# Performance work log

Measured on AMD Instinct MI355X. Metric: run time of the kernel, lower is better.

## Reference

```python
import math
import jax, jax.numpy as jnp
import numpy as np

EPS = 1e-5
NUM_HEADER = 2


def pos_encoding(C, T, dtype):
    i = jnp.arange(C)
    exp = -((i - (i % 2)).astype(dtype) / C)
    freqs = jnp.power(jnp.asarray(10000.0, dtype), exp)[:, None]      # [C,1]
    phases = ((i % 2).astype(dtype) * (np.pi / 2))[:, None]           # [C,1]
    pos = jnp.arange(T, dtype=dtype)[None, :]                         # [1,T]
    return jnp.sin(pos * freqs + phases)                              # [C,T]


def layernorm2d(x, g, b):
    # LayerNorm over (C,T) jointly, per batch element (nn.LayerNorm([C, length]))
    mu = jnp.mean(x, axis=(1, 2), keepdims=True)
    var = jnp.mean((x - mu) ** 2, axis=(1, 2), keepdims=True)
    return (x - mu) * jax.lax.rsqrt(var + EPS) * g[None] + b[None]


def dsconv(x, dw_w, dw_b, pw_w, pw_b):
    # depthwise conv1d (groups=C, 'same' padding for odd k) + pointwise 1x1
    C = x.shape[1]
    k = dw_w.shape[-1]
    y = jax.lax.conv_general_dilated(
        x, dw_w[:, None, :], (1,), [(k // 2, k // 2)],
        dimension_numbers=('NCH', 'OIH', 'NCH'), feature_group_count=C)
    y = y + dw_b[None, :, None]
    y = jnp.einsum('bct,oc->bot', y, pw_w) + pw_b[None, :, None]
    return y


def attention(x, mask, Wq, Wk, Wv, Wo):
    # Faithful to source bug: all heads use Wqs[1]/Wks[1]/Wvs[1] -> identical heads.
    xt = jnp.transpose(x, (0, 2, 1))          # [B,T,C]
    C = xt.shape[-1]
    dk = C / NUM_HEADER
    q = xt @ Wq                               # [B,T,dk]
    k_ = xt @ Wk
    v = xt @ Wv
    s = jnp.einsum('bqd,bkd->bqk', q, k_) * (1.0 / math.sqrt(dk))
    hmask = mask[:, None, :]                  # mask over keys
    s = s * hmask + (1 - hmask) * (-1e30)
    a = jax.nn.softmax(s, axis=2) * mask[:, :, None]
    head = a @ v                              # [B,T,dk]
    heads = jnp.tile(head, (1, 1, NUM_HEADER))  # concat of identical heads
    out = heads @ Wo                          # [B,T,C]
    return jnp.transpose(out, (0, 2, 1))      # [B,C,T]


def setup_inputs() -> dict:
    key = jax.random.key(0)
    B, C, T = 16, 128, 1024
    NCONV, K = 4, 7
    dk = C // NUM_HEADER
    ks = jax.random.split(key, 12)
    inp = {
        'x': jax.random.normal(ks[0], (B, C, T), jnp.float32),
        'mask': jnp.ones((B, T), jnp.float32),
        'dw_w': jax.random.normal(ks[1], (NCONV, C, K), jnp.float32) * math.sqrt(2.0 / K),
        'dw_b': jnp.zeros((NCONV, C), jnp.float32),
        'pw_w': jax.random.normal(ks[2], (NCONV, C, C), jnp.float32) * math.sqrt(2.0 / C),
        'pw_b': jnp.zeros((NCONV, C), jnp.float32),
        'norm0_g': jnp.ones((C, T), jnp.float32),
        'norm0_b': jnp.zeros((C, T), jnp.float32),
        'norms_g': jnp.ones((NCONV, C, T), jnp.float32),
        'norms_b': jnp.zeros((NCONV, C, T), jnp.float32),
        'norme_g': jnp.ones((C, T), jnp.float32),
        'norme_b': jnp.zeros((C, T), jnp.float32),
        'Wq': jax.random.normal(ks[3], (C, dk), jnp.float32) * math.sqrt(2.0 / (C + dk)),
        'Wk': jax.random.normal(ks[4], (C, dk), jnp.float32) * math.sqrt(2.0 / (C + dk)),
        'Wv': jax.random.normal(ks[5], (C, dk), jnp.float32) * math.sqrt(2.0 / (C + dk)),
        'Wo': jax.random.normal(ks[6], (C, C), jnp.float32) * math.sqrt(2.0 / C),
        'fc_w': jax.random.normal(ks[7], (C, C), jnp.float32) * (0.1 * math.sqrt(6.0 / (2 * C))),
        'fc_b': jnp.zeros((C,), jnp.float32),
    }
    return inp


def reference(x, mask, dw_w, dw_b, pw_w, pw_b, norm0_g, norm0_b,
              norms_g, norms_b, norme_g, norme_b,
              Wq, Wk, Wv, Wo, fc_w, fc_b):
    B, C, T = x.shape
    nconv = dw_w.shape[0]
    # dropout is identity in eval mode (reference is deterministic)
    out = x + pos_encoding(C, T, x.dtype)[None]
    res = layernorm2d(out, norm0_g, norm0_b)
    for i in range(nconv):
        out = dsconv(out, dw_w[i], dw_b[i], pw_w[i], pw_b[i])
        out = jax.nn.relu(out)
        out = out + res
        res = out
        out = layernorm2d(out, norms_g[i], norms_b[i])
    out = attention(out, mask, Wq, Wk, Wv, Wo)
    out = out + res
    res = out
    out = layernorm2d(out, norme_g, norme_b)
    out = jnp.einsum('bct,oc->bot', out, fc_w) + fc_b[None, :, None]
    out = jax.nn.relu(out)
    out = out + res
    return out
```

## Files before the change

kernel.cpp:

```cpp
#include <hip/hip_runtime.h>
#include <math.h>

#define BB 16
#define CC 128
#define TT 1024
#define KK 7
#define DK 64
#define NSPLIT 4

typedef float f32x4 __attribute__((ext_vector_type(4)));
typedef short s16x8 __attribute__((ext_vector_type(8)));

__device__ inline short f2bf(float f) {
  union { float f; unsigned u; } v; v.f = f;
  unsigned r = (v.u + 0x7FFFu + ((v.u >> 16) & 1u)) >> 16;
  return (short)r;
}

__device__ inline void block_partial_256(float s, float ss, float* dst) {
#pragma unroll
  for (int off = 32; off; off >>= 1) { s += __shfl_xor(s, off); ss += __shfl_xor(ss, off); }
  __shared__ float red[8];
  int w = threadIdx.x >> 6;
  if ((threadIdx.x & 63) == 0) { red[2 * w] = s; red[2 * w + 1] = ss; }
  __syncthreads();
  if (threadIdx.x == 0) {
    for (int i = 1; i < 4; ++i) { s += red[2 * i]; ss += red[2 * i + 1]; }
    dst[0] = s; dst[1] = ss;
  }
}

__device__ inline void ln_stats_from_parts(const float* part_batch, int n, float* sh) {
  if (threadIdx.x < 64) {
    float s = 0.f, ss = 0.f;
    for (int i = threadIdx.x; i < n; i += 64) { s += part_batch[2 * i]; ss += part_batch[2 * i + 1]; }
#pragma unroll
    for (int off = 32; off; off >>= 1) { s += __shfl_xor(s, off); ss += __shfl_xor(ss, off); }
    if (threadIdx.x == 0) {
      const float invN = 1.f / (float)(CC * TT);
      float mu = s * invN;
      sh[0] = mu;
      sh[1] = rsqrtf(ss * invN - mu * mu + 1e-5f);
    }
  }
  __syncthreads();
}

__global__ __launch_bounds__(256) void k_prep(const float* __restrict__ pww,
                                              const float* __restrict__ Wq,
                                              const float* __restrict__ Wk,
                                              const float* __restrict__ Wv,
                                              const float* __restrict__ Wo,
                                              const float* __restrict__ fcw,
                                              short* __restrict__ pwwb,
                                              short* __restrict__ wqkvb,
                                              short* __restrict__ wo2b,
                                              short* __restrict__ fcwb) {
  int i = blockIdx.x * 256 + threadIdx.x;
  if (i < 65536) { pwwb[i] = f2bf(pww[i]); return; }
  i -= 65536;
  if (i < 24576) {
    int m = i >> 7, c = i & 127;
    int sel = m >> 6, d = m & 63;
    const float* srcp = sel == 0 ? Wq : (sel == 1 ? Wk : Wv);
    wqkvb[i] = f2bf(srcp[c * DK + d]);
    return;
  }
  i -= 24576;
  if (i < 8192) {
    int o = i >> 6, d = i & 63;
    wo2b[i] = f2bf(Wo[d * CC + o] + Wo[(d + 64) * CC + o]);
    return;
  }
  i -= 8192;
  fcwb[i] = f2bf(fcw[i]);
}

__global__ __launch_bounds__(256) void k_addpos(const float* __restrict__ x,
                                                float* __restrict__ out,
                                                float* __restrict__ part) {
  int bc = blockIdx.x;
  int c = bc & (CC - 1);
  float ce = (float)(c & ~1);
  float freq = expf(-(ce / (float)CC) * 9.210340371976184f);
  float phase = (c & 1) ? 1.5707963267948966f : 0.0f;
  const float* xr = x + (size_t)bc * TT;
  float* orow = out + (size_t)bc * TT;
  float s = 0.f, ss = 0.f;
  for (int t = threadIdx.x; t < TT; t += 256) {
    float v = xr[t] + sinf((float)t * freq + phase);
    orow[t] = v;
    s += v; ss += v * v;
  }
  block_partial_256(s, ss, part + (size_t)bc * 2);
}

template <bool LN_IN, bool LN_RES>
__global__ __launch_bounds__(256) void k_dsconv(const float* __restrict__ in,
                                                const float* __restrict__ lng,
                                                const float* __restrict__ lnb,
                                                const float* __restrict__ part_in, int npart,
                                                const float* __restrict__ dww,
                                                const float* __restrict__ dwb,
                                                const short* __restrict__ pwwb,
                                                const float* __restrict__ pwb,
                                                float* __restrict__ out,
                                                float* __restrict__ part_out) {
  int tile = blockIdx.x & 31, b = blockIdx.x >> 5;
  int t0 = tile * 32;
  __shared__ float stats[2];
  __shared__ float xs[CC][39];
  __shared__ __align__(16) short Dt[32][136];
  ln_stats_from_parts(part_in + (size_t)b * npart * 2, npart, stats);
  float mu = stats[0], rs = stats[1];

  for (int i = threadIdx.x; i < CC * 38; i += 256) {
    int c = i / 38, j = i - c * 38;
    int t = t0 + j - 3;
    float v = 0.f;
    if (t >= 0 && t < TT) {
      v = in[((size_t)b * CC + c) * TT + t];
      if (LN_IN) v = (v - mu) * rs * lng[c * TT + t] + lnb[c * TT + t];
    }
    xs[c][j] = v;
  }
  __syncthreads();
  for (int i = threadIdx.x; i < 32 * CC; i += 256) {
    int t = i >> 7, c = i & 127;
    float a = dwb[c];
#pragma unroll
    for (int j = 0; j < KK; ++j) a += dww[c * KK + j] * xs[c][t + j];
    Dt[t][c] = f2bf(a);
  }
  __syncthreads();

  int w = threadIdx.x >> 6, lane = threadIdx.x & 63;
  int lo = lane & 15, hi = lane >> 4;
  f32x4 acc[2][2];
#pragma unroll
  for (int mt = 0; mt < 2; ++mt)
#pragma unroll
    for (int nt = 0; nt < 2; ++nt) { acc[mt][nt][0] = 0.f; acc[mt][nt][1] = 0.f; acc[mt][nt][2] = 0.f; acc[mt][nt][3] = 0.f; }
#pragma unroll
  for (int ks = 0; ks < 4; ++ks) {
    s16x8 b0 = *(const s16x8*)&Dt[lo][ks * 32 + hi * 8];
    s16x8 b1 = *(const s16x8*)&Dt[16 + lo][ks * 32 + hi * 8];
    s16x8 a0 = *(const s16x8*)&pwwb[(size_t)(w * 32 + lo) * CC + ks * 32 + hi * 8];
    s16x8 a1 = *(const s16x8*)&pwwb[(size_t)(w * 32 + 16 + lo) * CC + ks * 32 + hi * 8];
    acc[0][0] = __builtin_amdgcn_mfma_f32_16x16x32_bf16(a0, b0, acc[0][0], 0, 0, 0);
    acc[0][1] = __builtin_amdgcn_mfma_f32_16x16x32_bf16(a0, b1, acc[0][1], 0, 0, 0);
    acc[1][0] = __builtin_amdgcn_mfma_f32_16x16x32_bf16(a1, b0, acc[1][0], 0, 0, 0);
    acc[1][1] = __builtin_amdgcn_mfma_f32_16x16x32_bf16(a1, b1, acc[1][1], 0, 0, 0);
  }

  float s = 0.f, ss = 0.f;
#pragma unroll
  for (int mt = 0; mt < 2; ++mt)
#pragma unroll
    for (int nt = 0; nt < 2; ++nt)
#pragma unroll
      for (int r = 0; r < 4; ++r) {
        int row = w * 32 + mt * 16 + hi * 4 + r;
        int t = t0 + nt * 16 + lo;
        float v = acc[mt][nt][r] + pwb[row];
        v = v > 0.f ? v : 0.f;
        size_t idx = ((size_t)b * CC + row) * TT + t;
        float rv = in[idx];
        if (LN_RES) rv = (rv - mu) * rs * lng[row * TT + t] + lnb[row * TT + t];
        v += rv;
        out[idx] = v;
        s += v; ss += v * v;
      }
  block_partial_256(s, ss, part_out + (size_t)blockIdx.x * 2);
}

__global__ __launch_bounds__(256) void k_qkv(const float* __restrict__ in,
                                             const float* __restrict__ lng,
                                             const float* __restrict__ lnb,
                                             const float* __restrict__ part_in,
                                             const short* __restrict__ wqkvb,
                                             short* __restrict__ q,
                                             short* __restrict__ k,
                                             short* __restrict__ vt) {
  int tile = blockIdx.x & 31, b = blockIdx.x >> 5;
  int t0 = tile * 32;
  __shared__ float stats[2];
  __shared__ __align__(16) short Dt[32][136];
  ln_stats_from_parts(part_in + (size_t)b * 64, 32, stats);
  float mu = stats[0], rs = stats[1];
  for (int i = threadIdx.x; i < CC * 32; i += 256) {
    int c = i >> 5, t = i & 31;
    float v = in[((size_t)b * CC + c) * TT + t0 + t];
    Dt[t][c] = f2bf((v - mu) * rs * lng[c * TT + t0 + t] + lnb[c * TT + t0 + t]);
  }
  __syncthreads();

  int w = threadIdx.x >> 6, lane = threadIdx.x & 63;
  int lo = lane & 15, hi = lane >> 4;
  f32x4 acc[3][2];
#pragma unroll
  for (int mt = 0; mt < 3; ++mt)
#pragma unroll
    for (int nt = 0; nt < 2; ++nt) { acc[mt][nt][0] = 0.f; acc[mt][nt][1] = 0.f; acc[mt][nt][2] = 0.f; acc[mt][nt][3] = 0.f; }
#pragma unroll
  for (int ks = 0; ks < 4; ++ks) {
    s16x8 b0 = *(const s16x8*)&Dt[lo][ks * 32 + hi * 8];
    s16x8 b1 = *(const s16x8*)&Dt[16 + lo][ks * 32 + hi * 8];
#pragma unroll
    for (int mt = 0; mt < 3; ++mt) {
      s16x8 a = *(const s16x8*)&wqkvb[(size_t)(w * 48 + mt * 16 + lo) * CC + ks * 32 + hi * 8];
      acc[mt][0] = __builtin_amdgcn_mfma_f32_16x16x32_bf16(a, b0, acc[mt][0], 0, 0, 0);
      acc[mt][1] = __builtin_amdgcn_mfma_f32_16x16x32_bf16(a, b1, acc[mt][1], 0, 0, 0);
    }
  }
#pragma unroll
  for (int mt = 0; mt < 3; ++mt)
#pragma unroll
    for (int nt = 0; nt < 2; ++nt) {
      int m0 = w * 48 + mt * 16 + hi * 4;
      int t = t0 + nt * 16 + lo;
      short4 pk;
      pk.x = f2bf(acc[mt][nt][0]); pk.y = f2bf(acc[mt][nt][1]);
      pk.z = f2bf(acc[mt][nt][2]); pk.w = f2bf(acc[mt][nt][3]);
      if (m0 < 64) {
        *(short4*)(q + ((size_t)b * TT + t) * DK + m0) = pk;
      } else if (m0 < 128) {
        *(short4*)(k + ((size_t)b * TT + t) * DK + (m0 - 64)) = pk;
      } else {
        int d = m0 - 128;
        vt[((size_t)b * DK + d) * TT + t] = pk.x;
        vt[((size_t)b * DK + d + 1) * TT + t] = pk.y;
        vt[((size_t)b * DK + d + 2) * TT + t] = pk.z;
        vt[((size_t)b * DK + d + 3) * TT + t] = pk.w;
      }
    }
}

__global__ __launch_bounds__(128) void k_attn(const short* __restrict__ qb,
                                              const short* __restrict__ kbuf,
                                              const short* __restrict__ vtb,
                                              const float* __restrict__ mask,
                                              float* __restrict__ pacc,
                                              float* __restrict__ pml) {
  int sp = blockIdx.x & (NSPLIT - 1);
  int qt = (blockIdx.x >> 2) & 31;
  int b = blockIdx.x >> 7;
  int w = threadIdx.x >> 6, lane = threadIdx.x & 63;
  int lo = lane & 15, hi = lane >> 4;

  __shared__ __align__(16) short ks[64][72];
  __shared__ __align__(16) short vt[64][72];
  __shared__ __align__(16) short ps[2][16][68];
  __shared__ float ms[64];

  const short* qp = qb + ((size_t)b * TT + qt * 32 + w * 16 + lo) * DK + hi * 8;
  s16x8 aq0 = *(const s16x8*)qp;
  s16x8 aq1 = *(const s16x8*)(qp + 32);

  f32x4 acc[4];
  float m_i[4], l_i[4];
#pragma unroll
  for (int r = 0; r < 4; ++r) {
    m_i[r] = -3.0e38f; l_i[r] = 0.f;
#pragma unroll
    for (int nt = 0; nt < 4; ++nt) acc[nt][r] = 0.f;
  }
  const float scale = 0.125f;

  for (int kb2 = sp * (TT / 64 / NSPLIT); kb2 < (sp + 1) * (TT / 64 / NSPLIT); ++kb2) {
    __syncthreads();
    for (int i = threadIdx.x; i < 512; i += 128) {
      int r = i >> 3, ch = i & 7;
      *(s16x8*)&ks[r][ch * 8] =
          *(const s16x8*)(kbuf + ((size_t)b * TT + kb2 * 64 + r) * DK + ch * 8);
      *(s16x8*)&vt[r][ch * 8] =
          *(const s16x8*)(vtb + ((size_t)b * DK + r) * TT + kb2 * 64 + ch * 8);
    }
    if (threadIdx.x < 64) ms[threadIdx.x] = mask[(size_t)b * TT + kb2 * 64 + threadIdx.x];
    __syncthreads();

    f32x4 sc[4];
#pragma unroll
    for (int nt = 0; nt < 4; ++nt) {
      f32x4 z; z[0] = 0.f; z[1] = 0.f; z[2] = 0.f; z[3] = 0.f;
      s16x8 bk0 = *(const s16x8*)&ks[nt * 16 + lo][hi * 8];
      s16x8 bk1 = *(const s16x8*)&ks[nt * 16 + lo][32 + hi * 8];
      z = __builtin_amdgcn_mfma_f32_16x16x32_bf16(aq0, bk0, z, 0, 0, 0);
      z = __builtin_amdgcn_mfma_f32_16x16x32_bf16(aq1, bk1, z, 0, 0, 0);
      sc[nt] = z;
    }
#pragma unroll
    for (int nt = 0; nt < 4; ++nt) {
      float mv = ms[nt * 16 + lo];
      float addv = (1.f - mv) * -1e30f;
#pragma unroll
      for (int r = 0; r < 4; ++r) sc[nt][r] = sc[nt][r] * scale * mv + addv;
    }
    float alpha[4];
#pragma unroll
    for (int r = 0; r < 4; ++r) {
      float m0 = fmaxf(fmaxf(sc[0][r], sc[1][r]), fmaxf(sc[2][r], sc[3][r]));
#pragma unroll
      for (int off = 1; off < 16; off <<= 1) m0 = fmaxf(m0, __shfl_xor(m0, off));
      float mn = fmaxf(m_i[r], m0);
      alpha[r] = __expf(m_i[r] - mn);
      m_i[r] = mn;
    }
    float psum[4] = {0.f, 0.f, 0.f, 0.f};
#pragma unroll
    for (int nt = 0; nt < 4; ++nt)
#pragma unroll
      for (int r = 0; r < 4; ++r) {
        float p = __expf(sc[nt][r] - m_i[r]);
        psum[r] += p;
        ps[w][hi * 4 + r][nt * 16 + lo] = f2bf(p);
      }
#pragma unroll
    for (int r = 0; r < 4; ++r) {
      float sum = psum[r];
#pragma unroll
      for (int off = 1; off < 16; off <<= 1) sum += __shfl_xor(sum, off);
      l_i[r] = l_i[r] * alpha[r] + sum;
    }
#pragma unroll
    for (int nt = 0; nt < 4; ++nt)
#pragma unroll
      for (int r = 0; r < 4; ++r) acc[nt][r] *= alpha[r];

    s16x8 ap0 = *(const s16x8*)&ps[w][lo][hi * 8];
    s16x8 ap1 = *(const s16x8*)&ps[w][lo][32 + hi * 8];
#pragma unroll
    for (int nt = 0; nt < 4; ++nt) {
      s16x8 bv0 = *(const s16x8*)&vt[nt * 16 + lo][hi * 8];
      s16x8 bv1 = *(const s16x8*)&vt[nt * 16 + lo][32 + hi * 8];
      acc[nt] = __builtin_amdgcn_mfma_f32_16x16x32_bf16(ap0, bv0, acc[nt], 0, 0, 0);
      acc[nt] = __builtin_amdgcn_mfma_f32_16x16x32_bf16(ap1, bv1, acc[nt], 0, 0, 0);
    }
  }
#pragma unroll
  for (int r = 0; r < 4; ++r) {
    int row = qt * 32 + w * 16 + hi * 4 + r;
    size_t pb = (((size_t)b * TT + row) * NSPLIT + sp) * DK;
#pragma unroll
    for (int nt = 0; nt < 4; ++nt) pacc[pb + nt * 16 + lo] = acc[nt][r];
    if (lo == 0) {
      size_t mb = (((size_t)b * TT + row) * NSPLIT + sp) * 2;
      pml[mb] = m_i[r];
      pml[mb + 1] = l_i[r];
    }
  }
}

__global__ __launch_bounds__(256) void k_attn_combine(const float* __restrict__ pacc,
                                                      const float* __restrict__ pml,
                                                      const float* __restrict__ mask,
                                                      short* __restrict__ head) {
  int tid = blockIdx.x * 256 + threadIdx.x;
  int chunk = tid & 3;
  int row = (tid >> 2) & (TT - 1);
  int b = tid >> 12;
  size_t rb = (size_t)b * TT + row;
  float m[NSPLIT], l[NSPLIT];
#pragma unroll
  for (int s = 0; s < NSPLIT; ++s) {
    m[s] = pml[(rb * NSPLIT + s) * 2];
    l[s] = pml[(rb * NSPLIT + s) * 2 + 1];
  }
  float M = fmaxf(fmaxf(m[0], m[1]), fmaxf(m[2], m[3]));
  float wgt[NSPLIT], L = 0.f;
#pragma unroll
  for (int s = 0; s < NSPLIT; ++s) { wgt[s] = __expf(m[s] - M); L += wgt[s] * l[s]; }
  float inv = mask[rb] / L;
  float o[16];
#pragma unroll
  for (int j = 0; j < 16; ++j) o[j] = 0.f;
#pragma unroll
  for (int s = 0; s < NSPLIT; ++s) {
    const float4* pa = (const float4*)(pacc + (rb * NSPLIT + s) * DK + chunk * 16);
#pragma unroll
    for (int j4 = 0; j4 < 4; ++j4) {
      float4 v = pa[j4];
      o[j4 * 4] += wgt[s] * v.x; o[j4 * 4 + 1] += wgt[s] * v.y;
      o[j4 * 4 + 2] += wgt[s] * v.z; o[j4 * 4 + 3] += wgt[s] * v.w;
    }
  }
  short h[16];
#pragma unroll
  for (int j = 0; j < 16; ++j) h[j] = f2bf(o[j] * inv);
  *(uint4*)(head + rb * DK + chunk * 16) = *(uint4*)h;
  *(uint4*)(head + rb * DK + chunk * 16 + 8) = *(uint4*)(h + 8);
}

__global__ __launch_bounds__(256) void k_attnout(const short* __restrict__ head,
                                                 const short* __restrict__ wo2b,
                                                 const float* __restrict__ res,
                                                 float* __restrict__ out,
                                                 float* __restrict__ part_out) {
  int tile = blockIdx.x & 31, b = blockIdx.x >> 5;
  int t0 = tile * 32;
  __shared__ __align__(16) short Ht[32][72];
  {
    int i = threadIdx.x;
    int t = i >> 3, ch = i & 7;
    *(s16x8*)&Ht[t][ch * 8] =
        *(const s16x8*)(head + ((size_t)b * TT + t0 + t) * DK + ch * 8);
  }
  __syncthreads();

  int w = threadIdx.x >> 6, lane = threadIdx.x & 63;
  int lo = lane & 15, hi = lane >> 4;
  f32x4 acc[2][2];
#pragma unroll
  for (int mt = 0; mt < 2; ++mt)
#pragma unroll
    for (int nt = 0; nt < 2; ++nt) { acc[mt][nt][0] = 0.f; acc[mt][nt][1] = 0.f; acc[mt][nt][2] = 0.f; acc[mt][nt][3] = 0.f; }
#pragma unroll
  for (int ks = 0; ks < 2; ++ks) {
    s16x8 b0 = *(const s16x8*)&Ht[lo][ks * 32 + hi * 8];
    s16x8 b1 = *(const s16x8*)&Ht[16 + lo][ks * 32 + hi * 8];
    s16x8 a0 = *(const s16x8*)&wo2b[(size_t)(w * 32 + lo) * DK + ks * 32 + hi * 8];
    s16x8 a1 = *(const s16x8*)&wo2b[(size_t)(w * 32 + 16 + lo) * DK + ks * 32 + hi * 8];
    acc[0][0] = __builtin_amdgcn_mfma_f32_16x16x32_bf16(a0, b0, acc[0][0], 0, 0, 0);
    acc[0][1] = __builtin_amdgcn_mfma_f32_16x16x32_bf16(a0, b1, acc[0][1], 0, 0, 0);
    acc[1][0] = __builtin_amdgcn_mfma_f32_16x16x32_bf16(a1, b0, acc[1][0], 0, 0, 0);
    acc[1][1] = __builtin_amdgcn_mfma_f32_16x16x32_bf16(a1, b1, acc[1][1], 0, 0, 0);
  }
  float s = 0.f, ss = 0.f;
#pragma unroll
  for (int mt = 0; mt < 2; ++mt)
#pragma unroll
    for (int nt = 0; nt < 2; ++nt)
#pragma unroll
      for (int r = 0; r < 4; ++r) {
        int row = w * 32 + mt * 16 + hi * 4 + r;
        int t = t0 + nt * 16 + lo;
        size_t idx = ((size_t)b * CC + row) * TT + t;
        float v = acc[mt][nt][r] + res[idx];
        out[idx] = v;
        s += v; ss += v * v;
      }
  block_partial_256(s, ss, part_out + (size_t)blockIdx.x * 2);
}

__global__ __launch_bounds__(256) void k_fc(const float* __restrict__ in,
                                            const float* __restrict__ lng,
                                            const float* __restrict__ lnb,
                                            const float* __restrict__ part_in,
                                            const short* __restrict__ fcwb,
                                            const float* __restrict__ fb,
                                            float* __restrict__ out) {
  int tile = blockIdx.x & 31, b = blockIdx.x >> 5;
  int t0 = tile * 32;
  __shared__ float stats[2];
  __shared__ __align__(16) short Dt[32][136];
  ln_stats_from_parts(part_in + (size_t)b * 64, 32, stats);
  float mu = stats[0], rs = stats[1];
  for (int i = threadIdx.x; i < CC * 32; i += 256) {
    int c = i >> 5, t = i & 31;
    float v = in[((size_t)b * CC + c) * TT + t0 + t];
    Dt[t][c] = f2bf((v - mu) * rs * lng[c * TT + t0 + t] + lnb[c * TT + t0 + t]);
  }
  __syncthreads();

  int w = threadIdx.x >> 6, lane = threadIdx.x & 63;
  int lo = lane & 15, hi = lane >> 4;
  f32x4 acc[2][2];
#pragma unroll
  for (int mt = 0; mt < 2; ++mt)
#pragma unroll
    for (int nt = 0; nt < 2; ++nt) { acc[mt][nt][0] = 0.f; acc[mt][nt][1] = 0.f; acc[mt][nt][2] = 0.f; acc[mt][nt][3] = 0.f; }
#pragma unroll
  for (int ks = 0; ks < 4; ++ks) {
    s16x8 b0 = *(const s16x8*)&Dt[lo][ks * 32 + hi * 8];
    s16x8 b1 = *(const s16x8*)&Dt[16 + lo][ks * 32 + hi * 8];
    s16x8 a0 = *(const s16x8*)&fcwb[(size_t)(w * 32 + lo) * CC + ks * 32 + hi * 8];
    s16x8 a1 = *(const s16x8*)&fcwb[(size_t)(w * 32 + 16 + lo) * CC + ks * 32 + hi * 8];
    acc[0][0] = __builtin_amdgcn_mfma_f32_16x16x32_bf16(a0, b0, acc[0][0], 0, 0, 0);
    acc[0][1] = __builtin_amdgcn_mfma_f32_16x16x32_bf16(a0, b1, acc[0][1], 0, 0, 0);
    acc[1][0] = __builtin_amdgcn_mfma_f32_16x16x32_bf16(a1, b0, acc[1][0], 0, 0, 0);
    acc[1][1] = __builtin_amdgcn_mfma_f32_16x16x32_bf16(a1, b1, acc[1][1], 0, 0, 0);
  }
#pragma unroll
  for (int mt = 0; mt < 2; ++mt)
#pragma unroll
    for (int nt = 0; nt < 2; ++nt)
#pragma unroll
      for (int r = 0; r < 4; ++r) {
        int row = w * 32 + mt * 16 + hi * 4 + r;
        int t = t0 + nt * 16 + lo;
        size_t idx = ((size_t)b * CC + row) * TT + t;
        float v = acc[mt][nt][r] + fb[row];
        v = v > 0.f ? v : 0.f;
        out[idx] = v + in[idx];
      }
}

extern "C" void kernel_launch(void* const* d_in, const int* in_sizes, int n_in,
                              void* d_out, int out_size, void* d_ws, size_t ws_size,
                              hipStream_t stream) {
  const float* x    = (const float*)d_in[0];
  const float* mask = (const float*)d_in[1];
  const float* dww  = (const float*)d_in[2];
  const float* dwb  = (const float*)d_in[3];
  const float* pww  = (const float*)d_in[4];
  const float* pwb  = (const float*)d_in[5];
  const float* n0g  = (const float*)d_in[6];
  const float* n0b  = (const float*)d_in[7];
  const float* nsg  = (const float*)d_in[8];
  const float* nsb  = (const float*)d_in[9];
  const float* neg_ = (const float*)d_in[10];
  const float* neb  = (const float*)d_in[11];
  const float* Wq   = (const float*)d_in[12];
  const float* Wk   = (const float*)d_in[13];
  const float* Wv   = (const float*)d_in[14];
  const float* Wo   = (const float*)d_in[15];
  const float* fcw  = (const float*)d_in[16];
  const float* fcb  = (const float*)d_in[17];
  float* out = (float*)d_out;

  float* W = (float*)d_ws;
  const size_t NBCT = (size_t)BB * CC * TT;
  const size_t NBTD = (size_t)BB * TT * DK;
  const size_t CT = (size_t)CC * TT;
  float* O     = W;
  float* S     = W + NBCT;
  float* PART0 = W + 2 * NBCT;
  float* PARTS = PART0 + 4096;
  float* PACC  = PARTS + 5 * 1024;
  float* PML   = PACC + NBTD * NSPLIT;
  short* QB    = (short*)(PML + (size_t)BB * TT * NSPLIT * 2);
  short* KB    = QB + NBTD;
  short* VT    = KB + NBTD;
  short* HDB   = VT + NBTD;
  short* PWWB  = HDB + NBTD;
  short* WQKVB = PWWB + 65536;
  short* WO2B  = WQKVB + 24576;
  short* FCWB  = WO2B + 8192;

  k_prep<<<448, 256, 0, stream>>>(pww, Wq, Wk, Wv, Wo, fcw, PWWB, WQKVB, WO2B, FCWB);
  k_addpos<<<BB * CC, 256, 0, stream>>>(x, O, PART0);
  k_dsconv<false, true><<<BB * 32, 256, 0, stream>>>(
      O, n0g, n0b, PART0, 128, dww, dwb, PWWB, pwb, S, PARTS);
  k_dsconv<true, false><<<BB * 32, 256, 0, stream>>>(
      S, nsg + 0 * CT, nsb + 0 * CT, PARTS, 32,
      dww + 1 * CC * KK, dwb + 1 * CC, PWWB + 1 * CC * CC, pwb + 1 * CC, O, PARTS + 1024);
  k_dsconv<true, false><<<BB * 32, 256, 0, stream>>>(
      O, nsg + 1 * CT, nsb + 1 * CT, PARTS + 1024, 32,
      dww + 2 * CC * KK, dwb + 2 * CC, PWWB + 2 * CC * CC, pwb + 2 * CC, S, PARTS + 2048);
  k_dsconv<true, false><<<BB * 32, 256, 0, stream>>>(
      S, nsg + 2 * CT, nsb + 2 * CT, PARTS + 2048, 32,
      dww + 3 * CC * KK, dwb + 3 * CC, PWWB + 3 * CC * CC, pwb + 3 * CC, O, PARTS + 3072);
  k_qkv<<<BB * 32, 256, 0, stream>>>(O, nsg + 3 * CT, nsb + 3 * CT, PARTS + 3072,
                                     WQKVB, QB, KB, VT);
  k_attn<<<BB * 32 * NSPLIT, 128, 0, stream>>>(QB, KB, VT, mask, PACC, PML);
  k_attn_combine<<<BB * TT * 4 / 256, 256, 0, stream>>>(PACC, PML, mask, HDB);
  k_attnout<<<BB * 32, 256, 0, stream>>>(HDB, WO2B, O, S, PARTS + 4096);
  k_fc<<<BB * 32, 256, 0, stream>>>(S, neg_, neb, PARTS + 4096, FCWB, fcb, out);
}
```

Baseline: 218.6 us.

## Store intermediates and LN params in bf16, fuse attention combine into output projection

Switches the inter-kernel activation buffers (O/S), the attention partial accumulators, and the per-element LayerNorm gamma/beta copies to bf16, halving global memory traffic in the bandwidth-bound conv/LN kernels. The split-K attention combine kernel is folded into the attention output projection kernel, removing a launch and one round trip through memory. The prep kernel now also converts the LN parameters on every call, which adds work, and the bf16 residual stream reduces accuracy.

```diff
diff --git a/kernel.cpp b/kernel.cpp
--- a/kernel.cpp
+++ b/kernel.cpp
@@ -16,6 +16,11 @@
   unsigned r = (v.u + 0x7FFFu + ((v.u >> 16) & 1u)) >> 16;
   return (short)r;
 }
+__device__ inline float bf2f(short s) {
+  union { unsigned u; float f; } v;
+  v.u = ((unsigned)(unsigned short)s) << 16;
+  return v.f;
+}
 
 __device__ inline void block_partial_256(float s, float ss, float* dst) {
 #pragma unroll
@@ -52,10 +57,17 @@
                                               const float* __restrict__ Wv,
                                               const float* __restrict__ Wo,
                                               const float* __restrict__ fcw,
+                                              const float* __restrict__ n0g,
+                                              const float* __restrict__ n0b,
+                                              const float* __restrict__ nsg,
+                                              const float* __restrict__ nsb,
+                                              const float* __restrict__ neg_,
+                                              const float* __restrict__ neb,
                                               short* __restrict__ pwwb,
                                               short* __restrict__ wqkvb,
                                               short* __restrict__ wo2b,
-                                              short* __restrict__ fcwb) {
+                                              short* __restrict__ fcwb,
+                                              short* __restrict__ lnpb) {
   int i = blockIdx.x * 256 + threadIdx.x;
   if (i < 65536) { pwwb[i] = f2bf(pww[i]); return; }
   i -= 65536;
@@ -73,38 +85,53 @@
     return;
   }
   i -= 8192;
-  fcwb[i] = f2bf(fcw[i]);
+  if (i < 16384) { fcwb[i] = f2bf(fcw[i]); return; }
+  i -= 16384;
+  if (i >= 1572864) return;
+  const int CT = CC * TT;
+  float v;
+  if (i < CT) v = n0g[i];
+  else if (i < 2 * CT) v = n0b[i - CT];
+  else if (i < 6 * CT) v = nsg[i - 2 * CT];
+  else if (i < 10 * CT) v = nsb[i - 6 * CT];
+  else if (i < 11 * CT) v = neg_[i - 10 * CT];
+  else v = neb[i - 11 * CT];
+  lnpb[i] = f2bf(v);
 }
 
 __global__ __launch_bounds__(256) void k_addpos(const float* __restrict__ x,
-                                                float* __restrict__ out,
+                                                short* __restrict__ out,
                                                 float* __restrict__ part) {
   int bc = blockIdx.x;
   int c = bc & (CC - 1);
   float ce = (float)(c & ~1);
   float freq = expf(-(ce / (float)CC) * 9.210340371976184f);
   float phase = (c & 1) ? 1.5707963267948966f : 0.0f;
-  const float* xr = x + (size_t)bc * TT;
-  float* orow = out + (size_t)bc * TT;
-  float s = 0.f, ss = 0.f;
-  for (int t = threadIdx.x; t < TT; t += 256) {
-    float v = xr[t] + sinf((float)t * freq + phase);
-    orow[t] = v;
-    s += v; ss += v * v;
-  }
+  const float4* xr = (const float4*)(x + (size_t)bc * TT);
+  short* orow = out + (size_t)bc * TT;
+  int t = threadIdx.x * 4;
+  float4 xv = xr[threadIdx.x];
+  float v0 = xv.x + sinf((float)t * freq + phase);
+  float v1 = xv.y + sinf((float)(t + 1) * freq + phase);
+  float v2 = xv.z + sinf((float)(t + 2) * freq + phase);
+  float v3 = xv.w + sinf((float)(t + 3) * freq + phase);
+  float s = v0 + v1 + v2 + v3;
+  float ss = v0 * v0 + v1 * v1 + v2 * v2 + v3 * v3;
+  short4 o; o.x = f2bf(v0); o.y = f2bf(v1); o.z = f2bf(v2); o.w = f2bf(v3);
+  *(short4*)(orow + t) = o;
   block_partial_256(s, ss, part + (size_t)bc * 2);
 }
 
 template <bool LN_IN, bool LN_RES>
-__global__ __launch_bounds__(256) void k_dsconv(const float* __restrict__ in,
-                                                const float* __restrict__ lng,
-                                                const float* __restrict__ lnb,
+__global__ __launch_bounds__(256) void k_dsconv(const short* __restrict__ in,
+                                                const short* __restrict__ lng,
+                                                const short* __restrict__ lnb,
                                                 const float* __restrict__ part_in, int npart,
                                                 const float* __restrict__ dww,
                                                 const float* __restrict__ dwb,
                                                 const short* __restrict__ pwwb,
                                                 const float* __restrict__ pwb,
-                                                float* __restrict__ out,
+                                                short* __restrict__ out,
                                                 float* __restrict__ part_out) {
   int tile = blockIdx.x & 31, b = blockIdx.x >> 5;
   int t0 = tile * 32;
@@ -119,8 +146,8 @@
     int t = t0 + j - 3;
     float v = 0.f;
     if (t >= 0 && t < TT) {
-      v = in[((size_t)b * CC + c) * TT + t];
-      if (LN_IN) v = (v - mu) * rs * lng[c * TT + t] + lnb[c * TT + t];
+      v = bf2f(in[((size_t)b * CC + c) * TT + t]);
+      if (LN_IN) v = (v - mu) * rs * bf2f(lng[c * TT + t]) + bf2f(lnb[c * TT + t]);
     }
     xs[c][j] = v;
   }
@@ -165,18 +192,18 @@
         float v = acc[mt][nt][r] + pwb[row];
         v = v > 0.f ? v : 0.f;
         size_t idx = ((size_t)b * CC + row) * TT + t;
-        float rv = in[idx];
-        if (LN_RES) rv = (rv - mu) * rs * lng[row * TT + t] + lnb[row * TT + t];
+        float rv = bf2f(in[idx]);
+        if (LN_RES) rv = (rv - mu) * rs * bf2f(lng[row * TT + t]) + bf2f(lnb[row * TT + t]);
         v += rv;
-        out[idx] = v;
+        out[idx] = f2bf(v);
         s += v; ss += v * v;
       }
   block_partial_256(s, ss, part_out + (size_t)blockIdx.x * 2);
 }
 
-__global__ __launch_bounds__(256) void k_qkv(const float* __restrict__ in,
-                                             const float* __restrict__ lng,
-                                             const float* __restrict__ lnb,
+__global__ __launch_bounds__(256) void k_qkv(const short* __restrict__ in,
+                                             const short* __restrict__ lng,
+                                             const short* __restrict__ lnb,
                                              const float* __restrict__ part_in,
                                              const short* __restrict__ wqkvb,
                                              short* __restrict__ q,
@@ -188,10 +215,16 @@
   __shared__ __align__(16) short Dt[32][136];
   ln_stats_from_parts(part_in + (size_t)b * 64, 32, stats);
   float mu = stats[0], rs = stats[1];
-  for (int i = threadIdx.x; i < CC * 32; i += 256) {
-    int c = i >> 5, t = i & 31;
-    float v = in[((size_t)b * CC + c) * TT + t0 + t];
-    Dt[t][c] = f2bf((v - mu) * rs * lng[c * TT + t0 + t] + lnb[c * TT + t0 + t]);
+  for (int i = threadIdx.x; i < CC * 16; i += 256) {
+    int c = i >> 4, t2 = (i & 15) * 2;
+    size_t base = ((size_t)b * CC + c) * TT + t0 + t2;
+    unsigned u = *(const unsigned*)(in + base);
+    unsigned g = *(const unsigned*)(lng + c * TT + t0 + t2);
+    unsigned bb2 = *(const unsigned*)(lnb + c * TT + t0 + t2);
+    float v0 = (bf2f((short)(u & 0xFFFF)) - mu) * rs * bf2f((short)(g & 0xFFFF)) + bf2f((short)(bb2 & 0xFFFF));
+    float v1 = (bf2f((short)(u >> 16)) - mu) * rs * bf2f((short)(g >> 16)) + bf2f((short)(bb2 >> 16));
+    Dt[t2][c] = f2bf(v0);
+    Dt[t2 + 1][c] = f2bf(v1);
   }
   __syncthreads();
 
@@ -240,7 +273,7 @@
                                               const short* __restrict__ kbuf,
                                               const short* __restrict__ vtb,
                                               const float* __restrict__ mask,
-                                              float* __restrict__ pacc,
+                                              short* __restrict__ pacc,
                                               float* __restrict__ pml) {
   int sp = blockIdx.x & (NSPLIT - 1);
   int qt = (blockIdx.x >> 2) & 31;
@@ -342,7 +375,7 @@
     int row = qt * 32 + w * 16 + hi * 4 + r;
     size_t pb = (((size_t)b * TT + row) * NSPLIT + sp) * DK;
 #pragma unroll
-    for (int nt = 0; nt < 4; ++nt) pacc[pb + nt * 16 + lo] = acc[nt][r];
+    for (int nt = 0; nt < 4; ++nt) pacc[pb + nt * 16 + lo] = f2bf(acc[nt][r]);
     if (lo == 0) {
       size_t mb = (((size_t)b * TT + row) * NSPLIT + sp) * 2;
       pml[mb] = m_i[r];
@@ -351,59 +384,43 @@
   }
 }
 
-__global__ __launch_bounds__(256) void k_attn_combine(const float* __restrict__ pacc,
-                                                      const float* __restrict__ pml,
-                                                      const float* __restrict__ mask,
-                                                      short* __restrict__ head) {
-  int tid = blockIdx.x * 256 + threadIdx.x;
-  int chunk = tid & 3;
-  int row = (tid >> 2) & (TT - 1);
-  int b = tid >> 12;
-  size_t rb = (size_t)b * TT + row;
-  float m[NSPLIT], l[NSPLIT];
-#pragma unroll
-  for (int s = 0; s < NSPLIT; ++s) {
-    m[s] = pml[(rb * NSPLIT + s) * 2];
-    l[s] = pml[(rb * NSPLIT + s) * 2 + 1];
-  }
-  float M = fmaxf(fmaxf(m[0], m[1]), fmaxf(m[2], m[3]));
-  float wgt[NSPLIT], L = 0.f;
-#pragma unroll
-  for (int s = 0; s < NSPLIT; ++s) { wgt[s] = __expf(m[s] - M); L += wgt[s] * l[s]; }
-  float inv = mask[rb] / L;
-  float o[16];
-#pragma unroll
-  for (int j = 0; j < 16; ++j) o[j] = 0.f;
-#pragma unroll
-  for (int s = 0; s < NSPLIT; ++s) {
-    const float4* pa = (const float4*)(pacc + (rb * NSPLIT + s) * DK + chunk * 16);
-#pragma unroll
-    for (int j4 = 0; j4 < 4; ++j4) {
-      float4 v = pa[j4];
-      o[j4 * 4] += wgt[s] * v.x; o[j4 * 4 + 1] += wgt[s] * v.y;
-      o[j4 * 4 + 2] += wgt[s] * v.z; o[j4 * 4 + 3] += wgt[s] * v.w;
-    }
-  }
-  short h[16];
-#pragma unroll
-  for (int j = 0; j < 16; ++j) h[j] = f2bf(o[j] * inv);
-  *(uint4*)(head + rb * DK + chunk * 16) = *(uint4*)h;
-  *(uint4*)(head + rb * DK + chunk * 16 + 8) = *(uint4*)(h + 8);
-}
-
-__global__ __launch_bounds__(256) void k_attnout(const short* __restrict__ head,
+__global__ __launch_bounds__(256) void k_attnout(const short* __restrict__ pacc,
+                                                 const float* __restrict__ pml,
+                                                 const float* __restrict__ mask,
                                                  const short* __restrict__ wo2b,
-                                                 const float* __restrict__ res,
-                                                 float* __restrict__ out,
+                                                 const short* __restrict__ res,
+                                                 short* __restrict__ out,
                                                  float* __restrict__ part_out) {
   int tile = blockIdx.x & 31, b = blockIdx.x >> 5;
   int t0 = tile * 32;
   __shared__ __align__(16) short Ht[32][72];
   {
-    int i = threadIdx.x;
-    int t = i >> 3, ch = i & 7;
-    *(s16x8*)&Ht[t][ch * 8] =
-        *(const s16x8*)(head + ((size_t)b * TT + t0 + t) * DK + ch * 8);
+    int row = threadIdx.x >> 3, d8 = threadIdx.x & 7;
+    size_t rb = (size_t)b * TT + t0 + row;
+    float m[NSPLIT], l[NSPLIT];
+#pragma unroll
+    for (int s = 0; s < NSPLIT; ++s) {
+      m[s] = pml[(rb * NSPLIT + s) * 2];
+      l[s] = pml[(rb * NSPLIT + s) * 2 + 1];
+    }
+    float M = fmaxf(fmaxf(m[0], m[1]), fmaxf(m[2], m[3]));
+    float wgt[NSPLIT], L = 0.f;
+#pragma unroll
+    for (int s = 0; s < NSPLIT; ++s) { wgt[s] = __expf(m[s] - M); L += wgt[s] * l[s]; }
+    float inv = mask[rb] / L;
+    float o[8];
+#pragma unroll
+    for (int j = 0; j < 8; ++j) o[j] = 0.f;
+#pragma unroll
+    for (int s = 0; s < NSPLIT; ++s) {
+      s16x8 pv = *(const s16x8*)(pacc + (rb * NSPLIT + s) * DK + d8 * 8);
+#pragma unroll
+      for (int j = 0; j < 8; ++j) o[j] += wgt[s] * bf2f(pv[j]);
+    }
+    s16x8 hv;
+#pragma unroll
+    for (int j = 0; j < 8; ++j) hv[j] = f2bf(o[j] * inv);
+    *(s16x8*)&Ht[row][d8 * 8] = hv;
   }
   __syncthreads();
 
@@ -435,16 +452,16 @@
         int row = w * 32 + mt * 16 + hi * 4 + r;
         int t = t0 + nt * 16 + lo;
         size_t idx = ((size_t)b * CC + row) * TT + t;
-        float v = acc[mt][nt][r] + res[idx];
-        out[idx] = v;
+        float v = acc[mt][nt][r] + bf2f(res[idx]);
+        out[idx] = f2bf(v);
         s += v; ss += v * v;
       }
   block_partial_256(s, ss, part_out + (size_t)blockIdx.x * 2);
 }
 
-__global__ __launch_bounds__(256) void k_fc(const float* __restrict__ in,
-                                            const float* __restrict__ lng,
-                                            const float* __restrict__ lnb,
+__global__ __launch_bounds__(256) void k_fc(const short* __restrict__ in,
+                                            const short* __restrict__ lng,
+                                            const short* __restrict__ lnb,
                                             const float* __restrict__ part_in,
                                             const short* __restrict__ fcwb,
                                             const float* __restrict__ fb,
@@ -455,10 +472,16 @@
   __shared__ __align__(16) short Dt[32][136];
   ln_stats_from_parts(part_in + (size_t)b * 64, 32, stats);
   float mu = stats[0], rs = stats[1];
-  for (int i = threadIdx.x; i < CC * 32; i += 256) {
-    int c = i >> 5, t = i & 31;
-    float v = in[((size_t)b * CC + c) * TT + t0 + t];
-    Dt[t][c] = f2bf((v - mu) * rs * lng[c * TT + t0 + t] + lnb[c * TT + t0 + t]);
+  for (int i = threadIdx.x; i < CC * 16; i += 256) {
+    int c = i >> 4, t2 = (i & 15) * 2;
+    size_t base = ((size_t)b * CC + c) * TT + t0 + t2;
+    unsigned u = *(const unsigned*)(in + base);
+    unsigned g = *(const unsigned*)(lng + c * TT + t0 + t2);
+    unsigned bb2 = *(const unsigned*)(lnb + c * TT + t0 + t2);
+    float v0 = (bf2f((short)(u & 0xFFFF)) - mu) * rs * bf2f((short)(g & 0xFFFF)) + bf2f((short)(bb2 & 0xFFFF));
+    float v1 = (bf2f((short)(u >> 16)) - mu) * rs * bf2f((short)(g >> 16)) + bf2f((short)(bb2 >> 16));
+    Dt[t2][c] = f2bf(v0);
+    Dt[t2 + 1][c] = f2bf(v1);
   }
   __syncthreads();
 
@@ -491,7 +514,7 @@
         size_t idx = ((size_t)b * CC + row) * TT + t;
         float v = acc[mt][nt][r] + fb[row];
         v = v > 0.f ? v : 0.f;
-        out[idx] = v + in[idx];
+        out[idx] = v + bf2f(in[idx]);
       }
 }
 
@@ -522,38 +545,43 @@
   const size_t NBCT = (size_t)BB * CC * TT;
   const size_t NBTD = (size_t)BB * TT * DK;
   const size_t CT = (size_t)CC * TT;
-  float* O     = W;
-  float* S     = W + NBCT;
-  float* PART0 = W + 2 * NBCT;
-  float* PARTS = PART0 + 4096;
-  float* PACC  = PARTS + 5 * 1024;
-  float* PML   = PACC + NBTD * NSPLIT;
-  short* QB    = (short*)(PML + (size_t)BB * TT * NSPLIT * 2);
+  float* PART0 = W;
+  float* PARTS = W + 4096;
+  float* PML   = W + 9216;
+  short* OB    = (short*)(W + 140288);
+  short* SB    = OB + NBCT;
+  short* QB    = SB + NBCT;
   short* KB    = QB + NBTD;
   short* VT    = KB + NBTD;
-  short* HDB   = VT + NBTD;
-  short* PWWB  = HDB + NBTD;
+  short* PACC  = VT + NBTD;
+  short* PWWB  = PACC + NBTD * NSPLIT;
   short* WQKVB = PWWB + 65536;
   short* WO2B  = WQKVB + 24576;
   short* FCWB  = WO2B + 8192;
-
-  k_prep<<<448, 256, 0, stream>>>(pww, Wq, Wk, Wv, Wo, fcw, PWWB, WQKVB, WO2B, FCWB);
-  k_addpos<<<BB * CC, 256, 0, stream>>>(x, O, PART0);
+  short* LNPB  = FCWB + 16384;
+  short* N0G = LNPB, *N0B = LNPB + CT;
+  short* NSG0 = LNPB + 2 * CT;
+  short* NSB0 = LNPB + 6 * CT;
+  short* NEG = LNPB + 10 * CT, *NEB = LNPB + 11 * CT;
+
+  k_prep<<<6592, 256, 0, stream>>>(pww, Wq, Wk, Wv, Wo, fcw,
+                                   n0g, n0b, nsg, nsb, neg_, neb,
+                                   PWWB, WQKVB, WO2B, FCWB, LNPB);
+  k_addpos<<<BB * CC, 256, 0, stream>>>(x, OB, PART0);
   k_dsconv<false, true><<<BB * 32, 256, 0, stream>>>(
-      O, n0g, n0b, PART0, 128, dww, dwb, PWWB, pwb, S, PARTS);
+      OB, N0G, N0B, PART0, 128, dww, dwb, PWWB, pwb, SB, PARTS);
   k_dsconv<true, false><<<BB * 32, 256, 0, stream>>>(
-      S, nsg + 0 * CT, nsb + 0 * CT, PARTS, 32,
-      dww + 1 * CC * KK, dwb + 1 * CC, PWWB + 1 * CC * CC, pwb + 1 * CC, O, PARTS + 1024);
+      SB, NSG0, NSB0, PARTS, 32,
+      dww + 1 * CC * KK, dwb + 1 * CC, PWWB + 1 * CC * CC, pwb + 1 * CC, OB, PARTS + 1024);
   k_dsconv<true, false><<<BB * 32, 256, 0, stream>>>(
-      O, nsg + 1 * CT, nsb + 1 * CT, PARTS + 1024, 32,
-      dww + 2 * CC * KK, dwb + 2 * CC, PWWB + 2 * CC * CC, pwb + 2 * CC, S, PARTS + 2048);
+      OB, NSG0 + CT, NSB0 + CT, PARTS + 1024, 32,
+      dww + 2 * CC * KK, dwb + 2 * CC, PWWB + 2 * CC * CC, pwb + 2 * CC, SB, PARTS + 2048);
   k_dsconv<true, false><<<BB * 32, 256, 0, stream>>>(
-      S, nsg + 2 * CT, nsb + 2 * CT, PARTS + 2048, 32,
-      dww + 3 * CC * KK, dwb + 3 * CC, PWWB + 3 * CC * CC, pwb + 3 * CC, O, PARTS + 3072);
-  k_qkv<<<BB * 32, 256, 0, stream>>>(O, nsg + 3 * CT, nsb + 3 * CT, PARTS + 3072,
+      SB, NSG0 + 2 * CT, NSB0 + 2 * CT, PARTS + 2048, 32,
+      dww + 3 * CC * KK, dwb + 3 * CC, PWWB + 3 * CC * CC, pwb + 3 * CC, OB, PARTS + 3072);
+  k_qkv<<<BB * 32, 256, 0, stream>>>(OB, NSG0 + 3 * CT, NSB0 + 3 * CT, PARTS + 3072,
                                      WQKVB, QB, KB, VT);
   k_attn<<<BB * 32 * NSPLIT, 128, 0, stream>>>(QB, KB, VT, mask, PACC, PML);
-  k_attn_combine<<<BB * TT * 4 / 256, 256, 0, stream>>>(PACC, PML, mask, HDB);
-  k_attnout<<<BB * 32, 256, 0, stream>>>(HDB, WO2B, O, S, PARTS + 4096);
-  k_fc<<<BB * 32, 256, 0, stream>>>(S, neg_, neb, PARTS + 4096, FCWB, fcb, out);
-}
+  k_attnout<<<BB * 32, 256, 0, stream>>>(PACC, PML, mask, WO2B, OB, SB, PARTS + 4096);
+  k_fc<<<BB * 32, 256, 0, stream>>>(SB, NEG, NEB, PARTS + 4096, FCWB, fcb, out);
+}
```

Result: slower. 229.1 us (+4.8%).
